# Kernel tuning notes

Measured on AMD Instinct MI355X. Metric: run time of the kernel, lower is better.

The kernel has to match this reference:

```python
import jax, jax.numpy as jnp
import numpy as np

N_USER = 50000
N_ITEM = 50000
E = 600000
D = 128
H = 2 * D  # FFN hidden
LN_EPS = 1e-5


def _xavier(k, shape):
    lim = float(np.sqrt(6.0 / (shape[0] + shape[1])))
    return jax.random.uniform(k, shape, jnp.float32, -lim, lim)


def setup_inputs() -> dict:
    key = jax.random.key(0)
    ks = jax.random.split(key, 12)
    return {
        "feat_user": jax.random.normal(ks[0], (N_USER, D), jnp.float32),
        "feat_item": jax.random.normal(ks[1], (N_ITEM, D), jnp.float32),
        "W_u2i": _xavier(ks[2], (D, D)),
        "b_u2i": jnp.zeros((D,), jnp.float32),
        "W_i2u": _xavier(ks[3], (D, D)),
        "b_i2u": jnp.zeros((D,), jnp.float32),
        "self_w_user": _xavier(ks[4], (D, D)),
        "self_w_item": _xavier(ks[5], (D, D)),
        "ln_g_user": jnp.ones((D,), jnp.float32),
        "ln_b_user": jnp.zeros((D,), jnp.float32),
        "ln_g_item": jnp.ones((D,), jnp.float32),
        "ln_b_item": jnp.zeros((D,), jnp.float32),
        "ffn_w1": _xavier(ks[6], (D, H)),
        "ffn_b1": jnp.zeros((H,), jnp.float32),
        "ffn_w2": _xavier(ks[7], (H, D)),
        "ffn_b2": jnp.zeros((D,), jnp.float32),
        "src_u2i": jax.random.randint(ks[8], (E,), 0, N_USER, jnp.int32),
        "dst_u2i": jax.random.randint(ks[9], (E,), 0, N_ITEM, jnp.int32),
        "src_i2u": jax.random.randint(ks[10], (E,), 0, N_ITEM, jnp.int32),
        "dst_i2u": jax.random.randint(ks[11], (E,), 0, N_USER, jnp.int32),
    }


def _layer_norm(x, g, b):
    m = jnp.mean(x, axis=-1, keepdims=True)
    v = jnp.mean(jnp.square(x - m), axis=-1, keepdims=True)
    return (x - m) * jax.lax.rsqrt(v + LN_EPS) * g + b


def reference(feat_user, feat_item, W_u2i, b_u2i, W_i2u, b_i2u,
              self_w_user, self_w_item,
              ln_g_user, ln_b_user, ln_g_item, ln_b_item,
              ffn_w1, ffn_b1, ffn_w2, ffn_b2,
              src_u2i, dst_u2i, src_i2u, dst_i2u):
    # GraphConv(norm='none'): transform src feats, gather along edges, sum per dst, add bias.
    msg_item = jax.ops.segment_sum((feat_user @ W_u2i)[src_u2i], dst_u2i,
                                   num_segments=N_ITEM) + b_u2i
    msg_user = jax.ops.segment_sum((feat_item @ W_i2u)[src_i2u], dst_i2u,
                                   num_segments=N_USER) + b_i2u
    # self-loop weight + relation aggregation
    h_user = feat_user @ self_w_user + msg_user
    h_item = feat_item @ self_w_item + msg_item
    # LayerNorm -> ReLU -> residual
    h_user = jax.nn.relu(_layer_norm(h_user, ln_g_user, ln_b_user)) + feat_user
    h_item = jax.nn.relu(_layer_norm(h_item, ln_g_item, ln_b_item)) + feat_item
    # shared FFN (Linear -> ReLU -> Linear)
    def ffn(x):
        return jax.nn.relu(x @ ffn_w1 + ffn_b1) @ ffn_w2 + ffn_b2
    return ffn(h_user), ffn(h_item)
```

## Files before the change

kernel.cpp:

```cpp
#include <hip/hip_runtime.h>

typedef unsigned short u16;
typedef __attribute__((ext_vector_type(4))) float f32x4;
typedef __attribute__((ext_vector_type(8))) short bf16x8;

#define MAXB 512
#define BUK  256
#define EMAX 4096

__device__ __forceinline__ float bf2f(u16 u) {
    union { unsigned int i; float f; } v; v.i = ((unsigned int)u) << 16; return v.f;
}
__device__ __forceinline__ u16 f2bf(float f) {
    union { float f; unsigned int i; } v; v.f = f;
    unsigned int r = v.i + 0x7fffu + ((v.i >> 16) & 1u);
    return (u16)(r >> 16);
}
__device__ __forceinline__ void gload16(const void* g, void* l) {
    __builtin_amdgcn_global_load_lds(
        (const __attribute__((address_space(1))) unsigned int*)g,
        (__attribute__((address_space(3))) unsigned int*)l, 16, 0, 0);
}

#define MFMA_PROLOG \
    __shared__ __align__(16) u16 As[128 * 128]; \
    __shared__ __align__(16) u16 Ws[128 * 128]; \
    const int tid = threadIdx.x, w = tid >> 6, l = tid & 63; \
    const int wr = (w >> 1) * 64, wc = (w & 1) * 64; \
    const int quad = l >> 4, lan = l & 15; \
    f32x4 acc[4][4]; \
    _Pragma("unroll") for (int i = 0; i < 4; i++) \
    _Pragma("unroll") for (int j = 0; j < 4; j++) acc[i][j] = (f32x4){0.f,0.f,0.f,0.f};

__device__ __forceinline__ void mfma_stage(
    const u16* Ab, int sA, const u16* Wb, int sW, int m0, int n0,
    int w, int l, u16* As, u16* Ws)
{
#pragma unroll
    for (int it = 0; it < 8; it++) {
        int o = ((it * 4 + w) * 64 + l) * 16;
        int row = o >> 8, cb = o & 255;
        gload16(Ab + (size_t)(m0 + row) * sA + (cb >> 1), (char*)As + o);
        gload16(Wb + (size_t)(n0 + row) * sW + (cb >> 1), (char*)Ws + o);
    }
}

#define MFMA_COMPUTE \
    _Pragma("unroll") for (int kk = 0; kk < 4; kk++) { \
        bf16x8 af[4], bfr[4]; \
        _Pragma("unroll") for (int i = 0; i < 4; i++) \
            af[i] = *(const bf16x8*)&As[(wr + i*16 + lan)*128 + kk*32 + quad*8]; \
        _Pragma("unroll") for (int j = 0; j < 4; j++) \
            bfr[j] = *(const bf16x8*)&Ws[(wc + j*16 + lan)*128 + kk*32 + quad*8]; \
        _Pragma("unroll") for (int i = 0; i < 4; i++) \
        _Pragma("unroll") for (int j = 0; j < 4; j++) \
            acc[i][j] = __builtin_amdgcn_mfma_f32_16x16x32_bf16(af[i], bfr[j], acc[i][j], 0,0,0); \
    }

__global__ __launch_bounds__(256) void msg_k(
    const u16* __restrict__ S, const u16* __restrict__ fb,
    const u16* __restrict__ wUrel, const u16* __restrict__ wUself,
    const u16* __restrict__ wIrel, const u16* __restrict__ wIself,
    int NUp, u16* __restrict__ C)
{
    MFMA_PROLOG
    const int m0 = blockIdx.x * 128;
    const bool isU = m0 < NUp;
    const u16* W0 = isU ? wUrel : wIrel;
    const u16* W1 = isU ? wUself : wIself;

    mfma_stage(S, 128, W0, 128, m0, 0, w, l, As, Ws);
    __syncthreads();
    MFMA_COMPUTE
    __syncthreads();
    mfma_stage(fb, 128, W1, 128, m0, 0, w, l, As, Ws);
    __syncthreads();
    MFMA_COMPUTE

#pragma unroll
    for (int j = 0; j < 4; j++) {
        int col = wc + j * 16 + lan;
#pragma unroll
        for (int i = 0; i < 4; i++) {
            int row0 = m0 + wr + i * 16 + quad * 4;
#pragma unroll
            for (int r = 0; r < 4; r++)
                C[(size_t)(row0 + r) * 128 + col] = f2bf(acc[i][j][r]);
        }
    }
}

__global__ __launch_bounds__(256) void ffn1_k(
    const u16* __restrict__ h, const u16* __restrict__ W,
    const float* __restrict__ bias, u16* __restrict__ C)
{
    MFMA_PROLOG
    const int m0 = blockIdx.x * 128, n0 = blockIdx.y * 128;
    mfma_stage(h, 128, W, 128, m0, n0, w, l, As, Ws);
    __syncthreads();
    MFMA_COMPUTE

#pragma unroll
    for (int j = 0; j < 4; j++) {
        int col = n0 + wc + j * 16 + lan;
        float bb = bias[col];
#pragma unroll
        for (int i = 0; i < 4; i++) {
            int row0 = m0 + wr + i * 16 + quad * 4;
#pragma unroll
            for (int r = 0; r < 4; r++)
                C[(size_t)(row0 + r) * 256 + col] = f2bf(fmaxf(acc[i][j][r] + bb, 0.f));
        }
    }
}

__global__ __launch_bounds__(256) void ffn2_k(
    const u16* __restrict__ hid, const u16* __restrict__ W,
    const float* __restrict__ bias, float* __restrict__ out,
    int NU, int NUp, int NI)
{
    MFMA_PROLOG
    const int m0 = blockIdx.x * 128;
    mfma_stage(hid, 256, W, 256, m0, 0, w, l, As, Ws);
    __syncthreads();
    MFMA_COMPUTE
    __syncthreads();
    mfma_stage(hid + 128, 256, W + 128, 256, m0, 0, w, l, As, Ws);
    __syncthreads();
    MFMA_COMPUTE

#pragma unroll
    for (int j = 0; j < 4; j++) {
        int col = wc + j * 16 + lan;
        float bb = bias[col];
#pragma unroll
        for (int i = 0; i < 4; i++) {
            int row0 = m0 + wr + i * 16 + quad * 4;
#pragma unroll
            for (int r = 0; r < 4; r++) {
                int gr = row0 + r, orow;
                if (gr < NUp) { if (gr >= NU) continue; orow = gr; }
                else { int ir = gr - NUp; if (ir >= NI) continue; orow = NU + ir; }
                out[(size_t)orow * 128 + col] = acc[i][j][r] + bb;
            }
        }
    }
}

__global__ __launch_bounds__(256) void prep_k(
    const float* __restrict__ fu, const float* __restrict__ fi,
    u16* __restrict__ fb, u16* __restrict__ S,
    int nu4, int ni4, int NU, int NUp, int NI, int NIp,
    const float* __restrict__ w0, const float* __restrict__ w1,
    const float* __restrict__ w2, const float* __restrict__ w3,
    const float* __restrict__ w4, const float* __restrict__ w5,
    u16* __restrict__ o0, u16* __restrict__ o1, u16* __restrict__ o2,
    u16* __restrict__ o3, u16* __restrict__ o4, u16* __restrict__ o5,
    int* __restrict__ cnt, int NBUK)
{
    int t = blockIdx.x * 256 + threadIdx.x;
    int nc = nu4 + ni4;
    if (t < nc) {
        const float* X; u16* Y; int idx;
        if (t < nu4) { X = fu; Y = fb; idx = t; }
        else { X = fi; Y = fb + (size_t)NUp * 128; idx = t - nu4; }
        float4 v = ((const float4*)X)[idx];
        ((ushort4*)Y)[idx] = make_ushort4(f2bf(v.x), f2bf(v.y), f2bf(v.z), f2bf(v.w));
        return;
    }
    int u = t - nc;
    if (u < 131072) {
        const float* W; u16* O; int K, N, idx;
        if (u < 65536) {
            int s = u >> 14; idx = u & 16383; K = 128; N = 128;
            W = s == 0 ? w0 : s == 1 ? w1 : s == 2 ? w2 : w3;
            O = s == 0 ? o0 : s == 1 ? o1 : s == 2 ? o2 : o3;
        } else {
            int v2 = u - 65536; int s = v2 >> 15; idx = v2 & 32767;
            if (s == 0) { W = w4; O = o4; K = 128; N = 256; }
            else        { W = w5; O = o5; K = 256; N = 128; }
        }
        int k = idx / N, n = idx % N;
        O[n * K + k] = f2bf(W[idx]);
        return;
    }
    int u2 = u - 131072;
    int padrows = (NUp - NU) + (NIp - NI);
    int padw = padrows * 32;
    if (u2 < 2 * padw) {
        int arr = u2 / padw, k = u2 % padw;
        int prow = k >> 5, c4 = k & 31;
        int row = (prow < NUp - NU) ? (NU + prow) : (NUp + NI + (prow - (NUp - NU)));
        u16* B = arr ? fb : S;
        ((ushort4*)B)[(size_t)row * 32 + c4] = make_ushort4(0, 0, 0, 0);
        return;
    }
    int c = u2 - 2 * padw;
    if (c <= NBUK) cnt[c] = 0;
}

__global__ __launch_bounds__(256) void chist_k(
    const int* __restrict__ dst0, const int* __restrict__ dst1,
    int* __restrict__ cnt, int E, int NI, int NBUK)
{
    __shared__ int lh[MAXB];
    int t = threadIdx.x;
    for (int i = t; i < MAXB; i += 256) lh[i] = 0;
    __syncthreads();
    for (long long e = (long long)blockIdx.x * 256 + t; e < 2LL * E;
         e += (long long)gridDim.x * 256) {
        int row = (e < E) ? dst0[e] : NI + dst1[e - E];
        atomicAdd(&lh[row >> 8], 1);
    }
    __syncthreads();
    for (int i = t; i < NBUK; i += 256)
        if (lh[i]) atomicAdd(&cnt[i], lh[i]);
}

__global__ __launch_bounds__(512) void cscan_k(
    const int* __restrict__ cnt, int* __restrict__ crp, int* __restrict__ chead,
    int* __restrict__ rowptr, int NBUK, int NR)
{
    __shared__ int s[512];
    int t = threadIdx.x;
    int carry = 0;
    for (int base = 0; base < NBUK; base += 512) {
        int i = base + t;
        int v = (i < NBUK) ? cnt[i] : 0;
        s[t] = v;
        __syncthreads();
        for (int off = 1; off < 512; off <<= 1) {
            int x = (t >= off) ? s[t - off] : 0;
            __syncthreads();
            s[t] += x;
            __syncthreads();
        }
        int excl = s[t] - v + carry;
        if (i < NBUK) { crp[i] = excl; chead[i] = excl; }
        carry += s[511];
        __syncthreads();
    }
    if (t == 0) { crp[NBUK] = carry; rowptr[NR] = carry; }
}

__global__ __launch_bounds__(256) void cpart_k(
    const int* __restrict__ src0, const int* __restrict__ dst0,
    const int* __restrict__ src1, const int* __restrict__ dst1,
    int* __restrict__ chead, unsigned int* __restrict__ ebuf,
    int E, int NI, int NBUK)
{
    __shared__ int lh[MAXB], lb[MAXB], lo[MAXB];
    int t = threadIdx.x;
    long long total = 2LL * E;
    long long per = (total + gridDim.x - 1) / gridDim.x;
    long long r0 = (long long)blockIdx.x * per;
    long long r1 = r0 + per; if (r1 > total) r1 = total;

    for (int i = t; i < MAXB; i += 256) { lh[i] = 0; lo[i] = 0; }
    __syncthreads();
    for (long long e = r0 + t; e < r1; e += 256) {
        int row = (e < E) ? dst0[e] : NI + dst1[e - E];
        atomicAdd(&lh[row >> 8], 1);
    }
    __syncthreads();
    for (int i = t; i < NBUK; i += 256)
        if (lh[i]) lb[i] = atomicAdd(&chead[i], lh[i]);
    __syncthreads();
    for (long long e = r0 + t; e < r1; e += 256) {
        int row, src;
        if (e < E) { row = dst0[e]; src = src0[e]; }
        else       { row = NI + dst1[e - E]; src = src1[e - E]; }
        int bin = row >> 8;
        int off = atomicAdd(&lo[bin], 1);
        ebuf[lb[bin] + off] = ((unsigned int)(row & 255) << 16) | (unsigned int)src;
    }
}

__global__ __launch_bounds__(256) void fsort_k(
    const int* __restrict__ crp, const unsigned int* __restrict__ ebuf,
    int* __restrict__ rowptr, u16* __restrict__ eidx, int NR)
{
    __shared__ unsigned int ep[EMAX];
    __shared__ u16 ss[EMAX];
    __shared__ int h[BUK], hd[BUK];
    int b = blockIdx.x, t = threadIdx.x;
    int base = crp[b];
    int n = crp[b + 1] - base;
    if (n > EMAX) n = EMAX;

    for (int i = t; i < n; i += 256) ep[i] = ebuf[base + i];
    if (t < BUK) h[t] = 0;
    __syncthreads();
    for (int i = t; i < n; i += 256) atomicAdd(&h[ep[i] >> 16], 1);
    __syncthreads();
    int v = (t < BUK) ? h[t] : 0;
    for (int off = 1; off < 256; off <<= 1) {
        int x = (t >= off) ? h[t - off] : 0;
        __syncthreads();
        if (t < BUK) h[t] += x;
        __syncthreads();
    }
    int excl = (t < BUK) ? (h[t] - v) : 0;
    if (t < BUK) {
        int absrow = b * BUK + t;
        if (absrow < NR) rowptr[absrow] = base + excl;
        hd[t] = excl;
    }
    __syncthreads();
    for (int i = t; i < n; i += 256) {
        unsigned int p = ep[i];
        int pos = atomicAdd(&hd[p >> 16], 1);
        ss[pos] = (u16)(p & 0xffffu);
    }
    __syncthreads();
    for (int i = t; i < n; i += 256) eidx[base + i] = ss[i];
}

__global__ __launch_bounds__(256) void gather_k(
    const int* __restrict__ rowptr, const u16* __restrict__ eidx,
    const u16* __restrict__ fb, u16* __restrict__ S,
    int NI, int NR, int NUp)
{
    int row = blockIdx.x * 4 + (threadIdx.x >> 6);
    int l = threadIdx.x & 63;
    if (row >= NR) return;
    const u16* F = (row < NI) ? fb : fb + (size_t)NUp * 128;
    int srow = (row < NI) ? (NUp + row) : (row - NI);
    int start = rowptr[row], end = rowptr[row + 1];
    int sub = l >> 4, li = l & 15;

    float a[8];
#pragma unroll
    for (int k = 0; k < 8; k++) a[k] = 0.f;

    for (int j = start; j < end; j += 8) {
        int je0 = j + sub, je1 = j + 4 + sub;
        int c0 = je0 < end ? je0 : end - 1;
        int c1 = je1 < end ? je1 : end - 1;
        int s0 = eidx[c0], s1 = eidx[c1];
        uint4 v0 = *(const uint4*)(F + (size_t)s0 * 128 + li * 8);
        uint4 v1 = *(const uint4*)(F + (size_t)s1 * 128 + li * 8);
        unsigned int w0[4] = {v0.x, v0.y, v0.z, v0.w};
        unsigned int w1[4] = {v1.x, v1.y, v1.z, v1.w};
        if (je0 < end) {
#pragma unroll
            for (int p = 0; p < 4; p++) {
                a[2*p]   += bf2f((u16)(w0[p] & 0xffffu));
                a[2*p+1] += bf2f((u16)(w0[p] >> 16));
            }
        }
        if (je1 < end) {
#pragma unroll
            for (int p = 0; p < 4; p++) {
                a[2*p]   += bf2f((u16)(w1[p] & 0xffffu));
                a[2*p+1] += bf2f((u16)(w1[p] >> 16));
            }
        }
    }
#pragma unroll
    for (int k = 0; k < 8; k++) {
        a[k] += __shfl_xor(a[k], 16, 64);
        a[k] += __shfl_xor(a[k], 32, 64);
    }
    if (sub == 0) {
        uint4 o;
        o.x = ((unsigned int)f2bf(a[1]) << 16) | f2bf(a[0]);
        o.y = ((unsigned int)f2bf(a[3]) << 16) | f2bf(a[2]);
        o.z = ((unsigned int)f2bf(a[5]) << 16) | f2bf(a[4]);
        o.w = ((unsigned int)f2bf(a[7]) << 16) | f2bf(a[6]);
        *(uint4*)(S + (size_t)srow * 128 + li * 8) = o;
    }
}

__global__ __launch_bounds__(256) void lnf_k(
    const u16* __restrict__ msg, u16* __restrict__ fb,
    const float* __restrict__ bmU, const float* __restrict__ bmI,
    const float* __restrict__ gU, const float* __restrict__ bU,
    const float* __restrict__ gI, const float* __restrict__ bI,
    int NUp, int NRp)
{
    int row = blockIdx.x * 4 + (threadIdx.x >> 6);
    int lane = threadIdx.x & 63;
    if (row >= NRp) return;
    bool isU = row < NUp;
    const float* bm = isU ? bmU : bmI;
    const float* g  = isU ? gU : gI;
    const float* b  = isU ? bU : bI;
    size_t base = (size_t)row * 128;
    float x0 = bf2f(msg[base + lane])      + bm[lane];
    float x1 = bf2f(msg[base + 64 + lane]) + bm[64 + lane];
    float s = x0 + x1;
#pragma unroll
    for (int o = 32; o > 0; o >>= 1) s += __shfl_xor(s, o, 64);
    float mean = s * 0.0078125f;
    float d0 = x0 - mean, d1 = x1 - mean;
    float q = d0 * d0 + d1 * d1;
#pragma unroll
    for (int o = 32; o > 0; o >>= 1) q += __shfl_xor(q, o, 64);
    float inv = rsqrtf(q * 0.0078125f + 1e-5f);
    float y0 = fmaxf(fmaf(d0 * inv, g[lane],      b[lane]),      0.f) + bf2f(fb[base + lane]);
    float y1 = fmaxf(fmaf(d1 * inv, g[64 + lane], b[64 + lane]), 0.f) + bf2f(fb[base + 64 + lane]);
    fb[base + lane]      = f2bf(y0);
    fb[base + 64 + lane] = f2bf(y1);
}

extern "C" void kernel_launch(void* const* d_in, const int* in_sizes, int n_in,
                              void* d_out, int out_size, void* d_ws, size_t ws_size,
                              hipStream_t stream)
{
    const float* feat_user   = (const float*)d_in[0];
    const float* feat_item   = (const float*)d_in[1];
    const float* W_u2i       = (const float*)d_in[2];
    const float* b_u2i       = (const float*)d_in[3];
    const float* W_i2u       = (const float*)d_in[4];
    const float* b_i2u       = (const float*)d_in[5];
    const float* self_w_user = (const float*)d_in[6];
    const float* self_w_item = (const float*)d_in[7];
    const float* ln_g_user   = (const float*)d_in[8];
    const float* ln_b_user   = (const float*)d_in[9];
    const float* ln_g_item   = (const float*)d_in[10];
    const float* ln_b_item   = (const float*)d_in[11];
    const float* ffn_w1      = (const float*)d_in[12];
    const float* ffn_b1      = (const float*)d_in[13];
    const float* ffn_w2      = (const float*)d_in[14];
    const float* ffn_b2      = (const float*)d_in[15];
    const int* src_u2i       = (const int*)d_in[16];
    const int* dst_u2i       = (const int*)d_in[17];
    const int* src_i2u       = (const int*)d_in[18];
    const int* dst_i2u       = (const int*)d_in[19];

    const int NU = in_sizes[0] / 128;
    const int NI = in_sizes[1] / 128;
    const int E  = in_sizes[16];
    const int NR = NI + NU;
    const int NUp = (NU + 127) & ~127;
    const int NIp = (NI + 127) & ~127;
    const int NRp = NUp + NIp;
    const int NBUK = (NR + BUK - 1) / BUK;

    char* ws = (char*)d_ws;
    u16* S    = (u16*)ws;
    u16* msg  = S + (size_t)NRp * 128;
    u16* hid  = S;
    u16* fb   = msg + (size_t)NRp * 128;
    char* R2  = (char*)(fb + (size_t)NRp * 128);

    int* cnt    = (int*)R2;
    int* crp    = cnt + (NBUK + 1);
    int* chead  = crp + (NBUK + 1);
    int* rowptr = chead + NBUK;
    unsigned int* ebuf = (unsigned int*)(rowptr + NR + 1);
    u16* eidx   = (u16*)(ebuf + 2 * (size_t)E);
    u16* wts    = (u16*)(eidx + 2 * (size_t)E);
    u16* w_u2iT = wts;
    u16* w_i2uT = w_u2iT + 16384;
    u16* selfUT = w_i2uT + 16384;
    u16* selfIT = selfUT + 16384;
    u16* ffn1T  = selfIT + 16384;
    u16* ffn2T  = ffn1T + 32768;

    float* out = (float*)d_out;
    dim3 blk(256);
    const int nu4 = NU * 128 / 4, ni4 = NI * 128 / 4;
    const int padw = ((NUp - NU) + (NIp - NI)) * 32;
    const int prep_n = nu4 + ni4 + 131072 + 2 * padw + NBUK + 1;

    prep_k<<<dim3((prep_n + 255) / 256), blk, 0, stream>>>(
        feat_user, feat_item, fb, S, nu4, ni4, NU, NUp, NI, NIp,
        W_u2i, W_i2u, self_w_user, self_w_item, ffn_w1, ffn_w2,
        w_u2iT, w_i2uT, selfUT, selfIT, ffn1T, ffn2T, cnt, NBUK);

    chist_k<<<dim3(512), blk, 0, stream>>>(dst_u2i, dst_i2u, cnt, E, NI, NBUK);
    cscan_k<<<dim3(1), dim3(512), 0, stream>>>(cnt, crp, chead, rowptr, NBUK, NR);
    cpart_k<<<dim3(512), blk, 0, stream>>>(
        src_u2i, dst_u2i, src_i2u, dst_i2u, chead, ebuf, E, NI, NBUK);
    fsort_k<<<dim3(NBUK), blk, 0, stream>>>(crp, ebuf, rowptr, eidx, NR);

    gather_k<<<dim3((NR + 3) / 4), blk, 0, stream>>>(
        rowptr, eidx, fb, S, NI, NR, NUp);

    msg_k<<<dim3(NRp / 128), blk, 0, stream>>>(
        S, fb, w_i2uT, selfUT, w_u2iT, selfIT, NUp, msg);

    lnf_k<<<dim3((NRp + 3) / 4), blk, 0, stream>>>(
        msg, fb, b_i2u, b_u2i, ln_g_user, ln_b_user, ln_g_item, ln_b_item,
        NUp, NRp);

    ffn1_k<<<dim3(NRp / 128, 2), blk, 0, stream>>>(fb, ffn1T, ffn_b1, hid);

    ffn2_k<<<dim3(NRp / 128), blk, 0, stream>>>(
        hid, ffn2T, ffn_b2, out, NU, NUp, NI);
}
```

Measured before the change: 337.0 us.

## Fuse LayerNorm into message GEMM, fuse both FFN GEMMs, deepen gather unroll

```diff
diff --git a/kernel.cpp b/kernel.cpp
--- a/kernel.cpp
+++ b/kernel.cpp
@@ -22,30 +22,31 @@
         (__attribute__((address_space(3))) unsigned int*)l, 16, 0, 0);
 }
 
-#define MFMA_PROLOG \
-    __shared__ __align__(16) u16 As[128 * 128]; \
-    __shared__ __align__(16) u16 Ws[128 * 128]; \
+#define MFMA_VARS \
     const int tid = threadIdx.x, w = tid >> 6, l = tid & 63; \
     const int wr = (w >> 1) * 64, wc = (w & 1) * 64; \
-    const int quad = l >> 4, lan = l & 15; \
-    f32x4 acc[4][4]; \
+    const int quad = l >> 4, lan = l & 15; (void)tid;
+
+#define ACC_INIT(A) \
     _Pragma("unroll") for (int i = 0; i < 4; i++) \
-    _Pragma("unroll") for (int j = 0; j < 4; j++) acc[i][j] = (f32x4){0.f,0.f,0.f,0.f};
-
-__device__ __forceinline__ void mfma_stage(
-    const u16* Ab, int sA, const u16* Wb, int sW, int m0, int n0,
-    int w, int l, u16* As, u16* Ws)
-{
-#pragma unroll
-    for (int it = 0; it < 8; it++) {
-        int o = ((it * 4 + w) * 64 + l) * 16;
-        int row = o >> 8, cb = o & 255;
-        gload16(Ab + (size_t)(m0 + row) * sA + (cb >> 1), (char*)As + o);
-        gload16(Wb + (size_t)(n0 + row) * sW + (cb >> 1), (char*)Ws + o);
-    }
-}
-
-#define MFMA_COMPUTE \
+    _Pragma("unroll") for (int j = 0; j < 4; j++) A[i][j] = (f32x4){0.f,0.f,0.f,0.f};
+
+#define STAGE_AW(Aptr, sA, Wptr, sW) \
+    _Pragma("unroll") for (int it = 0; it < 8; it++) { \
+        int o = ((it * 4 + w) * 64 + l) * 16; \
+        int row = o >> 8, cb = o & 255; \
+        gload16((Aptr) + (size_t)row * (sA) + (cb >> 1), (char*)As + o); \
+        gload16((Wptr) + (size_t)row * (sW) + (cb >> 1), (char*)Ws + o); \
+    }
+
+#define STAGE_W(Wptr, sW) \
+    _Pragma("unroll") for (int it = 0; it < 8; it++) { \
+        int o = ((it * 4 + w) * 64 + l) * 16; \
+        int row = o >> 8, cb = o & 255; \
+        gload16((Wptr) + (size_t)row * (sW) + (cb >> 1), (char*)Ws + o); \
+    }
+
+#define COMPUTE(A) \
     _Pragma("unroll") for (int kk = 0; kk < 4; kk++) { \
         bf16x8 af[4], bfr[4]; \
         _Pragma("unroll") for (int i = 0; i < 4; i++) \
@@ -54,85 +55,162 @@
             bfr[j] = *(const bf16x8*)&Ws[(wc + j*16 + lan)*128 + kk*32 + quad*8]; \
         _Pragma("unroll") for (int i = 0; i < 4; i++) \
         _Pragma("unroll") for (int j = 0; j < 4; j++) \
-            acc[i][j] = __builtin_amdgcn_mfma_f32_16x16x32_bf16(af[i], bfr[j], acc[i][j], 0,0,0); \
-    }
-
-__global__ __launch_bounds__(256) void msg_k(
-    const u16* __restrict__ S, const u16* __restrict__ fb,
+            A[i][j] = __builtin_amdgcn_mfma_f32_16x16x32_bf16(af[i], bfr[j], A[i][j], 0,0,0); \
+    }
+
+__global__ __launch_bounds__(256) void msgln_k(
+    const u16* __restrict__ S, u16* __restrict__ fb,
     const u16* __restrict__ wUrel, const u16* __restrict__ wUself,
     const u16* __restrict__ wIrel, const u16* __restrict__ wIself,
-    int NUp, u16* __restrict__ C)
-{
-    MFMA_PROLOG
+    const float* __restrict__ bmU, const float* __restrict__ bmI,
+    const float* __restrict__ gU, const float* __restrict__ bU,
+    const float* __restrict__ gI, const float* __restrict__ bI,
+    int NUp)
+{
+    __shared__ __align__(16) u16 As[128 * 128];
+    __shared__ __align__(16) u16 Ws[128 * 128];
+    __shared__ float ps[128][2][2];
+    MFMA_VARS
     const int m0 = blockIdx.x * 128;
     const bool isU = m0 < NUp;
     const u16* W0 = isU ? wUrel : wIrel;
     const u16* W1 = isU ? wUself : wIself;
-
-    mfma_stage(S, 128, W0, 128, m0, 0, w, l, As, Ws);
-    __syncthreads();
-    MFMA_COMPUTE
-    __syncthreads();
-    mfma_stage(fb, 128, W1, 128, m0, 0, w, l, As, Ws);
-    __syncthreads();
-    MFMA_COMPUTE
-
+    const float* bm = isU ? bmU : bmI;
+    const float* g  = isU ? gU : gI;
+    const float* b  = isU ? bU : bI;
+
+    f32x4 acc[4][4];
+    ACC_INIT(acc)
+
+    STAGE_AW(S + (size_t)m0 * 128, 128, W0, 128)
+    __syncthreads();
+    COMPUTE(acc)
+    __syncthreads();
+    STAGE_AW(fb + (size_t)m0 * 128, 128, W1, 128)
+    __syncthreads();
+    COMPUTE(acc)
+
+    const int half = wc >> 6;
+    float bm4[4], g4[4], b4[4];
 #pragma unroll
     for (int j = 0; j < 4; j++) {
         int col = wc + j * 16 + lan;
-#pragma unroll
-        for (int i = 0; i < 4; i++) {
-            int row0 = m0 + wr + i * 16 + quad * 4;
-#pragma unroll
-            for (int r = 0; r < 4; r++)
-                C[(size_t)(row0 + r) * 128 + col] = f2bf(acc[i][j][r]);
-        }
-    }
-}
-
-__global__ __launch_bounds__(256) void ffn1_k(
-    const u16* __restrict__ h, const u16* __restrict__ W,
-    const float* __restrict__ bias, u16* __restrict__ C)
-{
-    MFMA_PROLOG
-    const int m0 = blockIdx.x * 128, n0 = blockIdx.y * 128;
-    mfma_stage(h, 128, W, 128, m0, n0, w, l, As, Ws);
-    __syncthreads();
-    MFMA_COMPUTE
-
+        bm4[j] = bm[col]; g4[j] = g[col]; b4[j] = b[col];
+    }
+#pragma unroll
+    for (int i = 0; i < 4; i++) {
+#pragma unroll
+        for (int r = 0; r < 4; r++) {
+            float s = 0.f, q = 0.f;
+#pragma unroll
+            for (int j = 0; j < 4; j++) {
+                float v = acc[i][j][r] + bm4[j];
+                s += v; q += v * v;
+            }
+#pragma unroll
+            for (int o = 1; o < 16; o <<= 1) {
+                s += __shfl_xor(s, o, 64);
+                q += __shfl_xor(q, o, 64);
+            }
+            if (lan == 0) {
+                int rl = wr + i * 16 + quad * 4 + r;
+                ps[rl][half][0] = s;
+                ps[rl][half][1] = q;
+            }
+        }
+    }
+    __syncthreads();
+#pragma unroll
+    for (int i = 0; i < 4; i++) {
+#pragma unroll
+        for (int r = 0; r < 4; r++) {
+            int rl = wr + i * 16 + quad * 4 + r;
+            float sum = ps[rl][0][0] + ps[rl][1][0];
+            float sq  = ps[rl][0][1] + ps[rl][1][1];
+            float mean = sum * 0.0078125f;
+            float var  = sq * 0.0078125f - mean * mean;
+            float inv  = rsqrtf(var + 1e-5f);
+#pragma unroll
+            for (int j = 0; j < 4; j++) {
+                int col = wc + j * 16 + lan;
+                float v = acc[i][j][r] + bm4[j];
+                float y = fmaxf(fmaf((v - mean) * inv, g4[j], b4[j]), 0.f)
+                          + bf2f(As[rl * 128 + col]);
+                fb[(size_t)(m0 + rl) * 128 + col] = f2bf(y);
+            }
+        }
+    }
+}
+
+__global__ __launch_bounds__(256) void ffn_k(
+    const u16* __restrict__ h, const u16* __restrict__ W1T,
+    const float* __restrict__ b1, const u16* __restrict__ W2T,
+    const float* __restrict__ b2, float* __restrict__ out,
+    int NU, int NUp, int NI)
+{
+    __shared__ __align__(16) u16 lds[2 * 128 * 128];
+    u16* As = lds;
+    u16* Ws = lds + 16384;
+    MFMA_VARS
+    const int m0 = blockIdx.x * 128;
+
+    f32x4 acc1[4][4], acc2[4][4];
+    ACC_INIT(acc1)
+    ACC_INIT(acc2)
+
+    STAGE_AW(h + (size_t)m0 * 128, 128, W1T, 128)
+    __syncthreads();
+    COMPUTE(acc1)
+    __syncthreads();
+    STAGE_W(W1T + (size_t)128 * 128, 128)
+    __syncthreads();
+    COMPUTE(acc2)
+    __syncthreads();
+
+    float b1a[4], b1b[4];
 #pragma unroll
     for (int j = 0; j < 4; j++) {
-        int col = n0 + wc + j * 16 + lan;
-        float bb = bias[col];
-#pragma unroll
-        for (int i = 0; i < 4; i++) {
-            int row0 = m0 + wr + i * 16 + quad * 4;
-#pragma unroll
-            for (int r = 0; r < 4; r++)
-                C[(size_t)(row0 + r) * 256 + col] = f2bf(fmaxf(acc[i][j][r] + bb, 0.f));
-        }
-    }
-}
-
-__global__ __launch_bounds__(256) void ffn2_k(
-    const u16* __restrict__ hid, const u16* __restrict__ W,
-    const float* __restrict__ bias, float* __restrict__ out,
-    int NU, int NUp, int NI)
-{
-    MFMA_PROLOG
-    const int m0 = blockIdx.x * 128;
-    mfma_stage(hid, 256, W, 256, m0, 0, w, l, As, Ws);
-    __syncthreads();
-    MFMA_COMPUTE
-    __syncthreads();
-    mfma_stage(hid + 128, 256, W + 128, 256, m0, 0, w, l, As, Ws);
-    __syncthreads();
-    MFMA_COMPUTE
+        b1a[j] = b1[wc + j * 16 + lan];
+        b1b[j] = b1[128 + wc + j * 16 + lan];
+    }
+    u16* H = lds;
+#pragma unroll
+    for (int i = 0; i < 4; i++) {
+#pragma unroll
+        for (int r = 0; r < 4; r++) {
+            int rl = wr + i * 16 + quad * 4 + r;
+#pragma unroll
+            for (int j = 0; j < 4; j++) {
+                int col = wc + j * 16 + lan;
+                H[rl * 256 + col]       = f2bf(fmaxf(acc1[i][j][r] + b1a[j], 0.f));
+                H[rl * 256 + 128 + col] = f2bf(fmaxf(acc2[i][j][r] + b1b[j], 0.f));
+            }
+        }
+    }
+    __syncthreads();
+
+    f32x4 acc3[4][4];
+    ACC_INIT(acc3)
+#pragma unroll
+    for (int kk = 0; kk < 8; kk++) {
+        bf16x8 af[4], bfr[4];
+#pragma unroll
+        for (int i = 0; i < 4; i++)
+            af[i] = *(const bf16x8*)&H[(wr + i * 16 + lan) * 256 + kk * 32 + quad * 8];
+#pragma unroll
+        for (int j = 0; j < 4; j++)
+            bfr[j] = *(const bf16x8*)&W2T[(size_t)(wc + j * 16 + lan) * 256 + kk * 32 + quad * 8];
+#pragma unroll
+        for (int i = 0; i < 4; i++)
+#pragma unroll
+            for (int j = 0; j < 4; j++)
+                acc3[i][j] = __builtin_amdgcn_mfma_f32_16x16x32_bf16(af[i], bfr[j], acc3[i][j], 0, 0, 0);
+    }
 
 #pragma unroll
     for (int j = 0; j < 4; j++) {
         int col = wc + j * 16 + lan;
-        float bb = bias[col];
+        float bb = b2[col];
 #pragma unroll
         for (int i = 0; i < 4; i++) {
             int row0 = m0 + wr + i * 16 + quad * 4;
@@ -141,7 +219,7 @@
                 int gr = row0 + r, orow;
                 if (gr < NUp) { if (gr >= NU) continue; orow = gr; }
                 else { int ir = gr - NUp; if (ir >= NI) continue; orow = NU + ir; }
-                out[(size_t)orow * 128 + col] = acc[i][j][r] + bb;
+                out[(size_t)orow * 128 + col] = acc3[i][j][r] + bb;
             }
         }
     }
@@ -333,27 +411,26 @@
 #pragma unroll
     for (int k = 0; k < 8; k++) a[k] = 0.f;
 
-    for (int j = start; j < end; j += 8) {
-        int je0 = j + sub, je1 = j + 4 + sub;
-        int c0 = je0 < end ? je0 : end - 1;
-        int c1 = je1 < end ? je1 : end - 1;
-        int s0 = eidx[c0], s1 = eidx[c1];
-        uint4 v0 = *(const uint4*)(F + (size_t)s0 * 128 + li * 8);
-        uint4 v1 = *(const uint4*)(F + (size_t)s1 * 128 + li * 8);
-        unsigned int w0[4] = {v0.x, v0.y, v0.z, v0.w};
-        unsigned int w1[4] = {v1.x, v1.y, v1.z, v1.w};
-        if (je0 < end) {
-#pragma unroll
-            for (int p = 0; p < 4; p++) {
-                a[2*p]   += bf2f((u16)(w0[p] & 0xffffu));
-                a[2*p+1] += bf2f((u16)(w0[p] >> 16));
-            }
-        }
-        if (je1 < end) {
-#pragma unroll
-            for (int p = 0; p < 4; p++) {
-                a[2*p]   += bf2f((u16)(w1[p] & 0xffffu));
-                a[2*p+1] += bf2f((u16)(w1[p] >> 16));
+    for (int j = start; j < end; j += 16) {
+        int idx[4]; uint4 v[4];
+#pragma unroll
+        for (int u = 0; u < 4; u++) {
+            int je = j + u * 4 + sub;
+            int c = je < end ? je : end - 1;
+            idx[u] = eidx[c];
+        }
+#pragma unroll
+        for (int u = 0; u < 4; u++)
+            v[u] = *(const uint4*)(F + (size_t)idx[u] * 128 + li * 8);
+#pragma unroll
+        for (int u = 0; u < 4; u++) {
+            if (j + u * 4 + sub < end) {
+                unsigned int ww[4] = {v[u].x, v[u].y, v[u].z, v[u].w};
+#pragma unroll
+                for (int p = 0; p < 4; p++) {
+                    a[2*p]   += bf2f((u16)(ww[p] & 0xffffu));
+                    a[2*p+1] += bf2f((u16)(ww[p] >> 16));
+                }
             }
         }
     }
@@ -370,38 +447,6 @@
         o.w = ((unsigned int)f2bf(a[7]) << 16) | f2bf(a[6]);
         *(uint4*)(S + (size_t)srow * 128 + li * 8) = o;
     }
-}
-
-__global__ __launch_bounds__(256) void lnf_k(
-    const u16* __restrict__ msg, u16* __restrict__ fb,
-    const float* __restrict__ bmU, const float* __restrict__ bmI,
-    const float* __restrict__ gU, const float* __restrict__ bU,
-    const float* __restrict__ gI, const float* __restrict__ bI,
-    int NUp, int NRp)
-{
-    int row = blockIdx.x * 4 + (threadIdx.x >> 6);
-    int lane = threadIdx.x & 63;
-    if (row >= NRp) return;
-    bool isU = row < NUp;
-    const float* bm = isU ? bmU : bmI;
-    const float* g  = isU ? gU : gI;
-    const float* b  = isU ? bU : bI;
-    size_t base = (size_t)row * 128;
-    float x0 = bf2f(msg[base + lane])      + bm[lane];
-    float x1 = bf2f(msg[base + 64 + lane]) + bm[64 + lane];
-    float s = x0 + x1;
-#pragma unroll
-    for (int o = 32; o > 0; o >>= 1) s += __shfl_xor(s, o, 64);
-    float mean = s * 0.0078125f;
-    float d0 = x0 - mean, d1 = x1 - mean;
-    float q = d0 * d0 + d1 * d1;
-#pragma unroll
-    for (int o = 32; o > 0; o >>= 1) q += __shfl_xor(q, o, 64);
-    float inv = rsqrtf(q * 0.0078125f + 1e-5f);
-    float y0 = fmaxf(fmaf(d0 * inv, g[lane],      b[lane]),      0.f) + bf2f(fb[base + lane]);
-    float y1 = fmaxf(fmaf(d1 * inv, g[64 + lane], b[64 + lane]), 0.f) + bf2f(fb[base + 64 + lane]);
-    fb[base + lane]      = f2bf(y0);
-    fb[base + 64 + lane] = f2bf(y1);
 }
 
 extern "C" void kernel_launch(void* const* d_in, const int* in_sizes, int n_in,
@@ -439,11 +484,9 @@
     const int NBUK = (NR + BUK - 1) / BUK;
 
     char* ws = (char*)d_ws;
-    u16* S    = (u16*)ws;
-    u16* msg  = S + (size_t)NRp * 128;
-    u16* hid  = S;
-    u16* fb   = msg + (size_t)NRp * 128;
-    char* R2  = (char*)(fb + (size_t)NRp * 128);
+    u16* S  = (u16*)ws;
+    u16* fb = S + (size_t)NRp * 128;
+    char* R2 = (char*)(fb + (size_t)NRp * 128);
 
     int* cnt    = (int*)R2;
     int* crp    = cnt + (NBUK + 1);
@@ -479,15 +522,10 @@
     gather_k<<<dim3((NR + 3) / 4), blk, 0, stream>>>(
         rowptr, eidx, fb, S, NI, NR, NUp);
 
-    msg_k<<<dim3(NRp / 128), blk, 0, stream>>>(
-        S, fb, w_i2uT, selfUT, w_u2iT, selfIT, NUp, msg);
-
-    lnf_k<<<dim3((NRp + 3) / 4), blk, 0, stream>>>(
-        msg, fb, b_i2u, b_u2i, ln_g_user, ln_b_user, ln_g_item, ln_b_item,
-        NUp, NRp);
-
-    ffn1_k<<<dim3(NRp / 128, 2), blk, 0, stream>>>(fb, ffn1T, ffn_b1, hid);
-
-    ffn2_k<<<dim3(NRp / 128), blk, 0, stream>>>(
-        hid, ffn2T, ffn_b2, out, NU, NUp, NI);
-}
+    msgln_k<<<dim3(NRp / 128), blk, 0, stream>>>(
+        S, fb, w_i2uT, selfUT, w_u2iT, selfIT,
+        b_i2u, b_u2i, ln_g_user, ln_b_user, ln_g_item, ln_b_item, NUp);
+
+    ffn_k<<<dim3(NRp / 128), blk, 0, stream>>>(
+        fb, ffn1T, ffn_b1, ffn2T, ffn_b2, out, NU, NUp, NI);
+}
```

Result: no change. 341.3 us (+1.3%).
